# Optimization experiments

Hardware: AMD Instinct MI355X
Metric: run time of the kernel (lower is better)

Reference implementation:

```python
import jax, jax.numpy as jnp
import numpy as np

EMBED_DIM = 768
NUM_HEADS = 12
HEAD_DIM = EMBED_DIM // NUM_HEADS
SCALE = HEAD_DIM ** -0.5


def setup_inputs() -> dict:
    key = jax.random.key(0)
    k1, k2, k3, k4, k5 = jax.random.split(key, 5)
    B, T = 8, 1024
    init = 0.02
    return {
        "hidden_states": jax.random.normal(k1, (B, T, EMBED_DIM), dtype=jnp.float32),
        "qkv_w": jax.random.normal(k2, (EMBED_DIM, 3 * EMBED_DIM), dtype=jnp.float32) * init,
        "qkv_b": jnp.zeros((3 * EMBED_DIM,), dtype=jnp.float32),
        "proj_w": jax.random.normal(k3, (EMBED_DIM, EMBED_DIM), dtype=jnp.float32) * init,
        "proj_b": jnp.zeros((EMBED_DIM,), dtype=jnp.float32),
    }


def reference(hidden_states, qkv_w, qkv_b, proj_w, proj_b):
    B, T, E = hidden_states.shape
    # fused QKV projection: [B, T, 3E] -> [3, B, H, T, Dh]
    mixed = hidden_states @ qkv_w + qkv_b
    mixed = mixed.reshape(B, T, 3, NUM_HEADS, HEAD_DIM).transpose(2, 0, 3, 1, 4)
    q, k, v = mixed[0], mixed[1], mixed[2]
    # scores: [B, H, T, T]
    scores = jnp.einsum("bhqd,bhkd->bhqk", q, k) * SCALE
    probs = jax.nn.softmax(scores, axis=-1)
    # context: [B, T, H, Dh] -> [B, T, E]
    ctx = jnp.einsum("bhqk,bhkd->bqhd", probs, v).reshape(B, T, E)
    return ctx @ proj_w + proj_b
```

## Files before the change

### kernel.cpp

```cpp
#include <hip/hip_runtime.h>
#include <hip/hip_bf16.h>

#define B_ 8
#define T_ 1024
#define E_ 768
#define H_ 12
#define DH_ 64
#define E3_ 2304
#define M_ (B_ * T_)
#define SCALE_LOG2E 0.18033688011112042f

typedef __attribute__((ext_vector_type(8))) short short8;
typedef __attribute__((ext_vector_type(4))) float float4_;
typedef __attribute__((ext_vector_type(4))) unsigned short ushort4_;

__device__ __forceinline__ unsigned short f2bf(float f) {
    union { float f; unsigned int u; } v; v.f = f;
    unsigned int r = v.u + 0x7fffu + ((v.u >> 16) & 1u);
    return (unsigned short)(r >> 16);
}

__device__ __forceinline__ unsigned int pk_bf16(float a, float b) {
    float2 t; t.x = a; t.y = b;
    union { __hip_bfloat162 h; unsigned int u; } cv;
    cv.h = __float22bfloat162_rn(t);
    return cv.u;
}

__device__ __forceinline__ void gld_lds16(const unsigned short* g, unsigned short* l) {
    __builtin_amdgcn_global_load_lds(
        (const __attribute__((address_space(1))) void*)g,
        (__attribute__((address_space(3))) void*)l,
        16, 0, 0);
}

__global__ __launch_bounds__(256) void prep(const float* __restrict__ hs,
                                            const float* __restrict__ qkv_w,
                                            const float* __restrict__ proj_w,
                                            unsigned short* __restrict__ hs_bf,
                                            unsigned short* __restrict__ qkvwT,
                                            unsigned short* __restrict__ projwT) {
    __shared__ float tile[32][33];
    const int id = blockIdx.x;
    const int tid = threadIdx.x;
    if (id < 6144) {
        const int i = (id * 256 + tid) * 4;
        float4_ v = *(const float4_*)(hs + i);
        ushort4_ o;
        o.x = f2bf(v.x); o.y = f2bf(v.y); o.z = f2bf(v.z); o.w = f2bf(v.w);
        *(ushort4_*)(hs_bf + i) = o;
        return;
    }
    const float* W; unsigned short* Wt; int N, bx, by;
    if (id < 6144 + 1728) {
        const int t = id - 6144; W = qkv_w; Wt = qkvwT; N = E3_;
        bx = t % 72; by = t / 72;
    } else {
        const int t = id - 7872; W = proj_w; Wt = projwT; N = E_;
        bx = t % 24; by = t / 24;
    }
    const int k0 = by * 32, n0 = bx * 32;
    const int tx = tid & 31, ty = tid >> 5;
    for (int i = ty; i < 32; i += 8)
        tile[i][tx] = W[(size_t)(k0 + i) * N + n0 + tx];
    __syncthreads();
    for (int i = ty; i < 32; i += 8)
        Wt[(size_t)(n0 + i) * E_ + k0 + tx] = f2bf(tile[tx][i]);
}

template <int STORE_MODE>
__global__ __launch_bounds__(256) void gemm_mfma(const unsigned short* __restrict__ A,
                                                 const unsigned short* __restrict__ Wt,
                                                 const float* __restrict__ bias,
                                                 void* __restrict__ Cout,
                                                 unsigned short* __restrict__ Vt,
                                                 int M, int N, int K) {
    __shared__ __align__(16) unsigned short Al[2][128 * 32];
    __shared__ __align__(16) unsigned short Wl[2][128 * 32];

    const int tid = threadIdx.x;
    const int lane = tid & 63;
    const int w = tid >> 6;

    const int id = blockIdx.x;
    const int xcd = id & 7;
    const int slot = id >> 3;
    const int bx = slot >> 3;
    const int by = xcd * 8 + (slot & 7);
    const int bm = by * 128;
    const int bn = bx * 128;

    const int wm = (w >> 1) * 64;
    const int wn = (w & 1) * 64;
    const int quad = lane >> 4;
    const int l16 = lane & 15;

    const int srow = w * 32 + (lane >> 2);
    const int schunk = (lane & 3) * 8;
    const int sbase = w * 32 * 32 + lane * 8;

    const unsigned short* ga = A + (size_t)(bm + srow) * K + schunk;
    const unsigned short* gw = Wt + (size_t)(bn + srow) * K + schunk;

    float4_ acc[4][4] = {};

    gld_lds16(ga, &Al[0][sbase]);
    gld_lds16(ga + (size_t)16 * K, &Al[0][sbase + 512]);
    gld_lds16(gw, &Wl[0][sbase]);
    gld_lds16(gw + (size_t)16 * K, &Wl[0][sbase + 512]);

    const int NI = K >> 5;
    for (int i = 0; i < NI; ++i) {
        const int cur = i & 1;
        __syncthreads();
        if (i + 1 < NI) {
            const unsigned short* ga2 = ga + (size_t)(i + 1) * 32;
            const unsigned short* gw2 = gw + (size_t)(i + 1) * 32;
            const int nxt = cur ^ 1;
            gld_lds16(ga2, &Al[nxt][sbase]);
            gld_lds16(ga2 + (size_t)16 * K, &Al[nxt][sbase + 512]);
            gld_lds16(gw2, &Wl[nxt][sbase]);
            gld_lds16(gw2 + (size_t)16 * K, &Wl[nxt][sbase + 512]);
        }
        short8 af[4], bf[4];
#pragma unroll
        for (int mt = 0; mt < 4; ++mt)
            af[mt] = *(const short8*)(&Al[cur][(wm + mt * 16 + l16) * 32 + quad * 8]);
#pragma unroll
        for (int nt = 0; nt < 4; ++nt)
            bf[nt] = *(const short8*)(&Wl[cur][(wn + nt * 16 + l16) * 32 + quad * 8]);
#pragma unroll
        for (int mt = 0; mt < 4; ++mt)
#pragma unroll
            for (int nt = 0; nt < 4; ++nt)
                acc[mt][nt] = __builtin_amdgcn_mfma_f32_16x16x32_bf16(af[mt], bf[nt],
                                                                      acc[mt][nt], 0, 0, 0);
    }

    {
#pragma unroll
        for (int nt = 0; nt < 4; ++nt) {
            const int col = bn + wn + nt * 16 + l16;
            const float bv = bias[col];
#pragma unroll
            for (int mt = 0; mt < 4; ++mt) {
#pragma unroll
                for (int i = 0; i < 4; ++i) {
                    const int row = bm + wm + mt * 16 + quad * 4 + i;
                    const float v = acc[mt][nt][i] + bv;
                    if (STORE_MODE >= 1)
                        ((unsigned short*)Cout)[(size_t)row * N + col] = f2bf(v);
                    else
                        ((float*)Cout)[(size_t)row * N + col] = v;
                }
            }
        }
    }
    (void)Vt;
}

__global__ __launch_bounds__(512, 2) void gemm288(const unsigned short* __restrict__ A,
                                                  const unsigned short* __restrict__ Wt,
                                                  const float* __restrict__ bias,
                                                  unsigned short* __restrict__ mixedOut,
                                                  unsigned short* __restrict__ Vt) {
    const int K = 768;
    const int NT = 12;
    __shared__ __align__(16) unsigned short lds[70144];

    const int tid = threadIdx.x;
    const int lane = tid & 63;
    const int w = tid >> 6;
    const int quad = lane >> 4;
    const int l16 = lane & 15;
    const int wM = w >> 1;
    const int wN = w & 1;

    const int id = blockIdx.x;
    const int xcd = id & 7;
    const int slot = id >> 3;
    const int bx = slot >> 2;
    const int byl = slot & 3;
    const int bm = (xcd * 4 + byl) * 256;
    const int bn = bx * 288;

    const int j4 = (w < 4) ? (w + 32) : 36;
    int kk0 = ((w % 18) / 6) * 64 + w;
    int kk1 = (((w + 8) % 18) / 6) * 64 + (w + 8);
    int kk2 = (((w + 16) % 18) / 6) * 64 + (w + 16);
    int kk3 = (((w + 24) % 18) / 6) * 64 + (w + 24);
    int kk4 = (j4 >= 36) ? (3 * 64 + 36) : (((j4 % 18) / 6) * 64 + j4);
#define CS_(a, b) { int _lo = min(a, b), _hi = max(a, b); a = _lo; b = _hi; }
    CS_(kk0, kk1) CS_(kk3, kk4) CS_(kk2, kk4) CS_(kk2, kk3) CS_(kk1, kk4)
    CS_(kk0, kk3) CS_(kk0, kk2) CS_(kk1, kk3) CS_(kk1, kk2)
#undef CS_
    const int b0 = kk0 & 63, b1 = kk1 & 63, b2 = kk2 & 63, b3 = kk3 & 63, b4 = kk4 & 63;

    const int srcrow = lane >> 3;
    const int ssw = ((lane & 7) ^ (srcrow & 7)) << 3;
    const unsigned short* gaL = A + (size_t)(bm + srcrow) * K + ssw;
    const unsigned short* gbL = Wt + (size_t)(bn + srcrow) * K + ssw;
    unsigned short* ldsl = lds + lane * 8;

    const int rsw0 = ((quad) ^ (l16 & 7)) << 3;
    const int rsw1 = ((quad + 4) ^ (l16 & 7)) << 3;
    const unsigned short* rdA = lds + (wM * 64 + l16) * 64;
    const unsigned short* rdB = lds + 32768 + (wN * 144 + l16) * 64;

    short8 aF[4][2], bF[3][2];
    float4_ acc[4][9] = {};

#define STA_(aj, toff, bufA) gld_lds16(gaL + (size_t)(aj) * 6144 + (toff), (bufA) + (aj) * 512)
#define STB_(j, toff, bufB) { \
    const int _j = (j); \
    const unsigned short* _s = gbL + (size_t)(_j >= 36 ? 0 : _j) * 6144 + (toff); \
    unsigned short* _d = (_j >= 36) ? (ldsl + 69632) : ((bufB) + _j * 512); \
    gld_lds16(_s, _d); }

#define LDA_(buf) { \
    const unsigned short* _a = rdA + (buf) * 16384; \
    aF[0][0] = *(const short8*)(_a + rsw0);        aF[0][1] = *(const short8*)(_a + rsw1); \
    aF[1][0] = *(const short8*)(_a + 1024 + rsw0); aF[1][1] = *(const short8*)(_a + 1024 + rsw1); \
    aF[2][0] = *(const short8*)(_a + 2048 + rsw0); aF[2][1] = *(const short8*)(_a + 2048 + rsw1); \
    aF[3][0] = *(const short8*)(_a + 3072 + rsw0); aF[3][1] = *(const short8*)(_a + 3072 + rsw1); }

#define LDB_(buf, nh) { \
    const unsigned short* _b = rdB + (buf) * 18432 + (nh) * 3072; \
    bF[0][0] = *(const short8*)(_b + rsw0);        bF[0][1] = *(const short8*)(_b + rsw1); \
    bF[1][0] = *(const short8*)(_b + 1024 + rsw0); bF[1][1] = *(const short8*)(_b + 1024 + rsw1); \
    bF[2][0] = *(const short8*)(_b + 2048 + rsw0); bF[2][1] = *(const short8*)(_b + 2048 + rsw1); }

#define MMA_(nh) \
    __builtin_amdgcn_s_setprio(1); \
    _Pragma("unroll") for (int mt = 0; mt < 4; ++mt) \
    _Pragma("unroll") for (int nt = 0; nt < 3; ++nt) { \
        acc[mt][(nh) * 3 + nt] = __builtin_amdgcn_mfma_f32_16x16x32_bf16( \
            aF[mt][0], bF[nt][0], acc[mt][(nh) * 3 + nt], 0, 0, 0); \
        acc[mt][(nh) * 3 + nt] = __builtin_amdgcn_mfma_f32_16x16x32_bf16( \
            aF[mt][1], bF[nt][1], acc[mt][(nh) * 3 + nt], 0, 0, 0); } \
    __builtin_amdgcn_s_setprio(0);

#define BARRIER_ __builtin_amdgcn_s_barrier()
#define WLGKM0_ { asm volatile("s_waitcnt lgkmcnt(0)" ::: "memory"); __builtin_amdgcn_sched_barrier(0); }
#define WVM3_ asm volatile("s_waitcnt vmcnt(3)" ::: "memory")
#define WVM0_ asm volatile("s_waitcnt vmcnt(0)" ::: "memory")

    {
        unsigned short* bufA = ldsl;
        unsigned short* bufB = ldsl + 32768;
        STA_(w, 0, bufA); STA_(w + 8, 0, bufA); STA_(w + 16, 0, bufA); STA_(w + 24, 0, bufA);
        STB_(b0, 0, bufB); STB_(b1, 0, bufB); STB_(b2, 0, bufB); STB_(b3, 0, bufB); STB_(b4, 0, bufB);
    }
    WVM3_; BARRIER_;

#pragma unroll 1
    for (int t = 0; t < NT - 1; ++t) {
        const int buf = t & 1;
        const int toff = (t + 1) * 64;
        unsigned short* bufA = ldsl + (buf ^ 1) * 16384;
        unsigned short* bufB = ldsl + 32768 + (buf ^ 1) * 18432;

        LDA_(buf); LDB_(buf, 0);
        STA_(w, toff, bufA); STA_(w + 8, toff, bufA); STA_(w + 16, toff, bufA);
        BARRIER_; WLGKM0_; MMA_(0);
        WVM3_; BARRIER_;
        LDB_(buf, 1);
        STA_(w + 24, toff, bufA); STB_(b0, toff, bufB); STB_(b1, toff, bufB);
        BARRIER_; WLGKM0_; MMA_(1);
        WVM3_; BARRIER_;
        LDB_(buf, 2);
        STB_(b2, toff, bufB); STB_(b3, toff, bufB); STB_(b4, toff, bufB);
        BARRIER_; WLGKM0_; MMA_(2);
        WVM3_; BARRIER_;
    }
    {
        LDA_(1); LDB_(1, 0);
        BARRIER_; WLGKM0_; MMA_(0);
        WVM0_; BARRIER_;
        LDB_(1, 1);
        BARRIER_; WLGKM0_; MMA_(1);
        BARRIER_;
        LDB_(1, 2);
        BARRIER_; WLGKM0_; MMA_(2);
    }
#undef STA_
#undef STB_
#undef LDA_
#undef LDB_
#undef MMA_

    const int bb = bm >> 10;
    const int tloc = (bm & 1023) + wM * 64;
#pragma unroll
    for (int ntg = 0; ntg < 9; ++ntg) {
        const int col = bn + wN * 144 + ntg * 16 + l16;
        const float bv = bias[col];
        if (col >= 1536) {
            const int n = col - 1536;
            const int h = n >> 6, d = n & 63;
            const size_t vrow = (size_t)((bb * H_ + h) * 64 + d) * T_;
#pragma unroll
            for (int mt = 0; mt < 4; ++mt) {
                uint2 pk;
                pk.x = pk_bf16(acc[mt][ntg][0] + bv, acc[mt][ntg][1] + bv);
                pk.y = pk_bf16(acc[mt][ntg][2] + bv, acc[mt][ntg][3] + bv);
                *(uint2*)(Vt + vrow + tloc + mt * 16 + quad * 4) = pk;
            }
        } else {
            const float qs = (col < 768) ? SCALE_LOG2E : 1.0f;
#pragma unroll
            for (int mt = 0; mt < 4; ++mt) {
#pragma unroll
                for (int i = 0; i < 4; ++i) {
                    const int row = bm + wM * 64 + mt * 16 + quad * 4 + i;
                    mixedOut[(size_t)row * E3_ + col] = f2bf((acc[mt][ntg][i] + bv) * qs);
                }
            }
        }
    }
}

__global__ __launch_bounds__(256) void attn_mfma(const unsigned short* __restrict__ mixed,
                                                 const unsigned short* __restrict__ Vt,
                                                 unsigned short* __restrict__ ctx) {
    const int bh = blockIdx.x;
    const int b = bh / H_;
    const int h = bh % H_;
    const int q0 = blockIdx.y * 128;
    const int tid = threadIdx.x;
    const int lane = tid & 63;
    const int w = tid >> 6;
    const int quad = lane >> 4;
    const int l16 = lane & 15;

    __shared__ __align__(16) unsigned short Kl[8 * 520];
    __shared__ __align__(16) unsigned short Vl[8 * 520];
    __shared__ __align__(16) unsigned short Pl[4][32 * 72];
    unsigned short* pw = &Pl[w][0];

    short8 qf[2][2];
#pragma unroll
    for (int hh = 0; hh < 2; ++hh) {
        const size_t qrow = (size_t)(b * T_ + q0 + w * 32 + hh * 16 + l16) * E3_ + h * 64;
        qf[hh][0] = *(const short8*)(mixed + qrow + quad * 8);
        qf[hh][1] = *(const short8*)(mixed + qrow + 32 + quad * 8);
    }

    float4_ o[2][4] = {};
    float lps[2] = {0.0f, 0.0f};

    const size_t kbase = (size_t)(b * T_) * E3_ + E_ + h * 64;
    const size_t vtb = (size_t)bh * 64 * T_;

    const int srow = tid >> 3;
    const int sc = tid & 7;

    short8 k1 = *(const short8*)(mixed + kbase + (size_t)srow * E3_ + sc * 8);
    short8 k2 = *(const short8*)(mixed + kbase + (size_t)(srow + 32) * E3_ + sc * 8);
    short8 v1 = *(const short8*)(Vt + vtb + (size_t)srow * T_ + sc * 8);
    short8 v2 = *(const short8*)(Vt + vtb + (size_t)(srow + 32) * T_ + sc * 8);

    for (int kv0 = 0; kv0 < T_; kv0 += 64) {
        __syncthreads();
        *(short8*)(&Kl[sc * 520 + srow * 8]) = k1;
        *(short8*)(&Kl[sc * 520 + (srow + 32) * 8]) = k2;
        *(short8*)(&Vl[sc * 520 + srow * 8]) = v1;
        *(short8*)(&Vl[sc * 520 + (srow + 32) * 8]) = v2;
        __syncthreads();

        if (kv0 + 64 < T_) {
            const int kn = kv0 + 64;
            k1 = *(const short8*)(mixed + kbase + (size_t)(kn + srow) * E3_ + sc * 8);
            k2 = *(const short8*)(mixed + kbase + (size_t)(kn + srow + 32) * E3_ + sc * 8);
            v1 = *(const short8*)(Vt + vtb + (size_t)srow * T_ + kn + sc * 8);
            v2 = *(const short8*)(Vt + vtb + (size_t)(srow + 32) * T_ + kn + sc * 8);
        }

        float4_ st[2][4];
#pragma unroll
        for (int nt = 0; nt < 4; ++nt) {
            const int key = nt * 16 + l16;
            short8 kf0 = *(const short8*)(&Kl[quad * 520 + key * 8]);
            short8 kf1 = *(const short8*)(&Kl[(4 + quad) * 520 + key * 8]);
#pragma unroll
            for (int hh = 0; hh < 2; ++hh) {
                float4_ z = {};
                z = __builtin_amdgcn_mfma_f32_16x16x32_bf16(kf0, qf[hh][0], z, 0, 0, 0);
                st[hh][nt] = __builtin_amdgcn_mfma_f32_16x16x32_bf16(kf1, qf[hh][1], z, 0, 0, 0);
            }
        }

#pragma unroll
        for (int hh = 0; hh < 2; ++hh) {
#pragma unroll
            for (int nt = 0; nt < 4; ++nt) {
                const float p0 = __builtin_amdgcn_exp2f(st[hh][nt][0]);
                const float p1 = __builtin_amdgcn_exp2f(st[hh][nt][1]);
                const float p2 = __builtin_amdgcn_exp2f(st[hh][nt][2]);
                const float p3 = __builtin_amdgcn_exp2f(st[hh][nt][3]);
                uint2 pk;
                pk.x = pk_bf16(p0, p1);
                pk.y = pk_bf16(p2, p3);
                lps[hh] += (p0 + p1) + (p2 + p3);
                *(uint2*)(&pw[(hh * 16 + l16) * 72 + nt * 16 + quad * 4]) = pk;
            }
        }

        short8 pf[2][2];
#pragma unroll
        for (int hh = 0; hh < 2; ++hh) {
            pf[hh][0] = *(const short8*)(&pw[(hh * 16 + l16) * 72 + quad * 8]);
            pf[hh][1] = *(const short8*)(&pw[(hh * 16 + l16) * 72 + 32 + quad * 8]);
        }

#pragma unroll
        for (int dt = 0; dt < 4; ++dt) {
            const int d = dt * 16 + l16;
            short8 vf0 = *(const short8*)(&Vl[quad * 520 + d * 8]);
            short8 vf1 = *(const short8*)(&Vl[(4 + quad) * 520 + d * 8]);
#pragma unroll
            for (int hh = 0; hh < 2; ++hh) {
                o[hh][dt] = __builtin_amdgcn_mfma_f32_16x16x32_bf16(pf[hh][0], vf0, o[hh][dt], 0, 0, 0);
                o[hh][dt] = __builtin_amdgcn_mfma_f32_16x16x32_bf16(pf[hh][1], vf1, o[hh][dt], 0, 0, 0);
            }
        }
    }

#pragma unroll
    for (int hh = 0; hh < 2; ++hh) {
        float l = lps[hh];
        l += __shfl_xor(l, 16, 64);
        l += __shfl_xor(l, 32, 64);
        float4_ inv;
#pragma unroll
        for (int i = 0; i < 4; ++i)
            inv[i] = 1.0f / __shfl(l, quad * 4 + i, 16);
#pragma unroll
        for (int dt = 0; dt < 4; ++dt) {
#pragma unroll
            for (int i = 0; i < 4; ++i) {
                const float v = o[hh][dt][i] * inv[i];
                const size_t row = (size_t)(b * T_ + q0 + w * 32 + hh * 16 + quad * 4 + i);
                ctx[row * E_ + h * 64 + dt * 16 + l16] = f2bf(v);
            }
        }
    }
}

extern "C" void kernel_launch(void* const* d_in, const int* in_sizes, int n_in,
                              void* d_out, int out_size, void* d_ws, size_t ws_size,
                              hipStream_t stream) {
    const float* hs     = (const float*)d_in[0];
    const float* qkv_w  = (const float*)d_in[1];
    const float* qkv_b  = (const float*)d_in[2];
    const float* proj_w = (const float*)d_in[3];
    const float* proj_b = (const float*)d_in[4];
    float* out = (float*)d_out;

    unsigned short* hs_bf  = (unsigned short*)d_ws;
    unsigned short* qkvwT  = hs_bf + (size_t)M_ * E_;
    unsigned short* projwT = qkvwT + (size_t)E3_ * E_;
    unsigned short* mixed  = projwT + (size_t)E_ * E_;
    unsigned short* Vt     = mixed + (size_t)M_ * E3_;
    unsigned short* ctx    = hs_bf;

    prep<<<8448, 256, 0, stream>>>(hs, qkv_w, proj_w, hs_bf, qkvwT, projwT);

    gemm288<<<256, 512, 0, stream>>>(hs_bf, qkvwT, qkv_b, mixed, Vt);
    attn_mfma<<<dim3(B_ * H_, T_ / 128), 256, 0, stream>>>(mixed, Vt, ctx);
    gemm_mfma<0><<<(E_ / 128) * (M_ / 128), 256, 0, stream>>>(ctx, projwT, proj_b,
                                                              (void*)out, nullptr, M_, E_, E_);
}
```

Before: 179.8 us.

## Switch attention to 32x32x16 MFMA and keep P in registers via permlane swap

Rewrites the attention inner loop to use 32x32x16 bf16 MFMAs, computing S^T so that each lane holds probabilities for one query column. The P tile is converted to the A-operand layout in registers with v_permlane32_swap instead of a round trip through shared memory, which removes the per-wave P buffer and its LDS writes and reads. This cuts LDS traffic and instruction count. In exchange it relies on exact register layout correctness for the swap and changes the epilogue's row mapping.

```diff
diff --git a/kernel.cpp b/kernel.cpp
--- a/kernel.cpp
+++ b/kernel.cpp
@@ -12,6 +12,7 @@
 
 typedef __attribute__((ext_vector_type(8))) short short8;
 typedef __attribute__((ext_vector_type(4))) float float4_;
+typedef __attribute__((ext_vector_type(16))) float f32x16;
 typedef __attribute__((ext_vector_type(4))) unsigned short ushort4_;
 
 __device__ __forceinline__ unsigned short f2bf(float f) {
@@ -25,6 +26,10 @@
     union { __hip_bfloat162 h; unsigned int u; } cv;
     cv.h = __float22bfloat162_rn(t);
     return cv.u;
+}
+
+__device__ __forceinline__ void pl32swap(unsigned int& a, unsigned int& b) {
+    asm volatile("v_permlane32_swap_b32 %0, %1" : "+v"(a), "+v"(b));
 }
 
 __device__ __forceinline__ void gld_lds16(const unsigned short* g, unsigned short* l) {
@@ -330,24 +335,23 @@
     const int tid = threadIdx.x;
     const int lane = tid & 63;
     const int w = tid >> 6;
-    const int quad = lane >> 4;
-    const int l16 = lane & 15;
+    const int l32 = lane & 31;
+    const int hi = lane >> 5;
 
     __shared__ __align__(16) unsigned short Kl[8 * 520];
     __shared__ __align__(16) unsigned short Vl[8 * 520];
-    __shared__ __align__(16) unsigned short Pl[4][32 * 72];
-    unsigned short* pw = &Pl[w][0];
-
-    short8 qf[2][2];
-#pragma unroll
-    for (int hh = 0; hh < 2; ++hh) {
-        const size_t qrow = (size_t)(b * T_ + q0 + w * 32 + hh * 16 + l16) * E3_ + h * 64;
-        qf[hh][0] = *(const short8*)(mixed + qrow + quad * 8);
-        qf[hh][1] = *(const short8*)(mixed + qrow + 32 + quad * 8);
-    }
-
-    float4_ o[2][4] = {};
-    float lps[2] = {0.0f, 0.0f};
+
+    short8 qB[4];
+    {
+        const size_t qrow = (size_t)(b * T_ + q0 + w * 32 + l32) * E3_ + h * 64;
+#pragma unroll
+        for (int dc = 0; dc < 4; ++dc)
+            qB[dc] = *(const short8*)(mixed + qrow + dc * 16 + hi * 8);
+    }
+
+    f32x16 o0 = {};
+    f32x16 o1 = {};
+    float lps = 0.0f;
 
     const size_t kbase = (size_t)(b * T_) * E3_ + E_ + h * 64;
     const size_t vtb = (size_t)bh * 64 * T_;
@@ -376,74 +380,63 @@
             v2 = *(const short8*)(Vt + vtb + (size_t)(srow + 32) * T_ + kn + sc * 8);
         }
 
-        float4_ st[2][4];
-#pragma unroll
-        for (int nt = 0; nt < 4; ++nt) {
-            const int key = nt * 16 + l16;
-            short8 kf0 = *(const short8*)(&Kl[quad * 520 + key * 8]);
-            short8 kf1 = *(const short8*)(&Kl[(4 + quad) * 520 + key * 8]);
-#pragma unroll
-            for (int hh = 0; hh < 2; ++hh) {
-                float4_ z = {};
-                z = __builtin_amdgcn_mfma_f32_16x16x32_bf16(kf0, qf[hh][0], z, 0, 0, 0);
-                st[hh][nt] = __builtin_amdgcn_mfma_f32_16x16x32_bf16(kf1, qf[hh][1], z, 0, 0, 0);
-            }
+#pragma unroll
+        for (int kg = 0; kg < 2; ++kg) {
+            short8 kf0 = *(const short8*)(&Kl[(0 + hi) * 520 + (kg * 32 + l32) * 8]);
+            short8 kf1 = *(const short8*)(&Kl[(2 + hi) * 520 + (kg * 32 + l32) * 8]);
+            short8 kf2 = *(const short8*)(&Kl[(4 + hi) * 520 + (kg * 32 + l32) * 8]);
+            short8 kf3 = *(const short8*)(&Kl[(6 + hi) * 520 + (kg * 32 + l32) * 8]);
+
+            f32x16 st = {};
+            st = __builtin_amdgcn_mfma_f32_32x32x16_bf16(kf0, qB[0], st, 0, 0, 0);
+            st = __builtin_amdgcn_mfma_f32_32x32x16_bf16(kf1, qB[1], st, 0, 0, 0);
+            st = __builtin_amdgcn_mfma_f32_32x32x16_bf16(kf2, qB[2], st, 0, 0, 0);
+            st = __builtin_amdgcn_mfma_f32_32x32x16_bf16(kf3, qB[3], st, 0, 0, 0);
+
+            float e[16];
+#pragma unroll
+            for (int r = 0; r < 16; ++r)
+                e[r] = __builtin_amdgcn_exp2f(st[r]);
+            lps += ((((e[0] + e[1]) + (e[2] + e[3])) + ((e[4] + e[5]) + (e[6] + e[7]))) +
+                    (((e[8] + e[9]) + (e[10] + e[11])) + ((e[12] + e[13]) + (e[14] + e[15]))));
+
+            unsigned int u0 = pk_bf16(e[0], e[1]);
+            unsigned int u1 = pk_bf16(e[2], e[3]);
+            unsigned int u2 = pk_bf16(e[4], e[5]);
+            unsigned int u3 = pk_bf16(e[6], e[7]);
+            pl32swap(u0, u2);
+            pl32swap(u1, u3);
+            unsigned int u4 = pk_bf16(e[8], e[9]);
+            unsigned int u5 = pk_bf16(e[10], e[11]);
+            unsigned int u6 = pk_bf16(e[12], e[13]);
+            unsigned int u7 = pk_bf16(e[14], e[15]);
+            pl32swap(u4, u6);
+            pl32swap(u5, u7);
+            union { unsigned int u[4]; short8 s; } pa0, pa1;
+            pa0.u[0] = u0; pa0.u[1] = u1; pa0.u[2] = u2; pa0.u[3] = u3;
+            pa1.u[0] = u4; pa1.u[1] = u5; pa1.u[2] = u6; pa1.u[3] = u7;
+
+            short8 vb00 = *(const short8*)(&Vl[(kg * 4 + 0 + hi) * 520 + l32 * 8]);
+            short8 vb01 = *(const short8*)(&Vl[(kg * 4 + 0 + hi) * 520 + (32 + l32) * 8]);
+            short8 vb10 = *(const short8*)(&Vl[(kg * 4 + 2 + hi) * 520 + l32 * 8]);
+            short8 vb11 = *(const short8*)(&Vl[(kg * 4 + 2 + hi) * 520 + (32 + l32) * 8]);
+
+            o0 = __builtin_amdgcn_mfma_f32_32x32x16_bf16(pa0.s, vb00, o0, 0, 0, 0);
+            o1 = __builtin_amdgcn_mfma_f32_32x32x16_bf16(pa0.s, vb01, o1, 0, 0, 0);
+            o0 = __builtin_amdgcn_mfma_f32_32x32x16_bf16(pa1.s, vb10, o0, 0, 0, 0);
+            o1 = __builtin_amdgcn_mfma_f32_32x32x16_bf16(pa1.s, vb11, o1, 0, 0, 0);
         }
-
-#pragma unroll
-        for (int hh = 0; hh < 2; ++hh) {
-#pragma unroll
-            for (int nt = 0; nt < 4; ++nt) {
-                const float p0 = __builtin_amdgcn_exp2f(st[hh][nt][0]);
-                const float p1 = __builtin_amdgcn_exp2f(st[hh][nt][1]);
-                const float p2 = __builtin_amdgcn_exp2f(st[hh][nt][2]);
-                const float p3 = __builtin_amdgcn_exp2f(st[hh][nt][3]);
-                uint2 pk;
-                pk.x = pk_bf16(p0, p1);
-                pk.y = pk_bf16(p2, p3);
-                lps[hh] += (p0 + p1) + (p2 + p3);
-                *(uint2*)(&pw[(hh * 16 + l16) * 72 + nt * 16 + quad * 4]) = pk;
-            }
-        }
-
-        short8 pf[2][2];
-#pragma unroll
-        for (int hh = 0; hh < 2; ++hh) {
-            pf[hh][0] = *(const short8*)(&pw[(hh * 16 + l16) * 72 + quad * 8]);
-            pf[hh][1] = *(const short8*)(&pw[(hh * 16 + l16) * 72 + 32 + quad * 8]);
-        }
-
-#pragma unroll
-        for (int dt = 0; dt < 4; ++dt) {
-            const int d = dt * 16 + l16;
-            short8 vf0 = *(const short8*)(&Vl[quad * 520 + d * 8]);
-            short8 vf1 = *(const short8*)(&Vl[(4 + quad) * 520 + d * 8]);
-#pragma unroll
-            for (int hh = 0; hh < 2; ++hh) {
-                o[hh][dt] = __builtin_amdgcn_mfma_f32_16x16x32_bf16(pf[hh][0], vf0, o[hh][dt], 0, 0, 0);
-                o[hh][dt] = __builtin_amdgcn_mfma_f32_16x16x32_bf16(pf[hh][1], vf1, o[hh][dt], 0, 0, 0);
-            }
-        }
-    }
-
-#pragma unroll
-    for (int hh = 0; hh < 2; ++hh) {
-        float l = lps[hh];
-        l += __shfl_xor(l, 16, 64);
-        l += __shfl_xor(l, 32, 64);
-        float4_ inv;
-#pragma unroll
-        for (int i = 0; i < 4; ++i)
-            inv[i] = 1.0f / __shfl(l, quad * 4 + i, 16);
-#pragma unroll
-        for (int dt = 0; dt < 4; ++dt) {
-#pragma unroll
-            for (int i = 0; i < 4; ++i) {
-                const float v = o[hh][dt][i] * inv[i];
-                const size_t row = (size_t)(b * T_ + q0 + w * 32 + hh * 16 + quad * 4 + i);
-                ctx[row * E_ + h * 64 + dt * 16 + l16] = f2bf(v);
-            }
-        }
+    }
+
+    const float lt = lps + __shfl_xor(lps, 32, 64);
+    const float invq = 1.0f / lt;
+#pragma unroll
+    for (int r = 0; r < 16; ++r) {
+        const int row = (r & 3) + 8 * (r >> 2) + 4 * hi;
+        const float iv = __shfl(invq, row, 32);
+        const size_t orow = (size_t)(b * T_ + q0 + w * 32 + row) * E_ + h * 64 + l32;
+        ctx[orow] = f2bf(o0[r] * iv);
+        ctx[orow + 32] = f2bf(o1[r] * iv);
     }
 }
 
```

Result: no change. 180.2 us (+0.2%).

## Replace output projection GEMM with 256x96-tiled pipelined kernel

Applied to the files above, without the earlier changes.

Replaces the generic 128x128 double-buffered output-projection GEMM with a dedicated kernel that uses 256x96 tiles, 512 threads and K-steps of 64. It adds XOR-swizzled LDS layout, staged async global-to-LDS loads interleaved with MFMA phases, and s_setprio around the MFMA bursts. The grid shrinks to 256 blocks, about one per CU, to cut wave-quantization and tail effects from the earlier 384-block launch. The cost is more complex hand-scheduled synchronization and higher register and LDS pressure.

```diff
diff --git a/kernel.cpp b/kernel.cpp
--- a/kernel.cpp
+++ b/kernel.cpp
@@ -68,97 +68,6 @@
         Wt[(size_t)(n0 + i) * E_ + k0 + tx] = f2bf(tile[tx][i]);
 }
 
-template <int STORE_MODE>
-__global__ __launch_bounds__(256) void gemm_mfma(const unsigned short* __restrict__ A,
-                                                 const unsigned short* __restrict__ Wt,
-                                                 const float* __restrict__ bias,
-                                                 void* __restrict__ Cout,
-                                                 unsigned short* __restrict__ Vt,
-                                                 int M, int N, int K) {
-    __shared__ __align__(16) unsigned short Al[2][128 * 32];
-    __shared__ __align__(16) unsigned short Wl[2][128 * 32];
-
-    const int tid = threadIdx.x;
-    const int lane = tid & 63;
-    const int w = tid >> 6;
-
-    const int id = blockIdx.x;
-    const int xcd = id & 7;
-    const int slot = id >> 3;
-    const int bx = slot >> 3;
-    const int by = xcd * 8 + (slot & 7);
-    const int bm = by * 128;
-    const int bn = bx * 128;
-
-    const int wm = (w >> 1) * 64;
-    const int wn = (w & 1) * 64;
-    const int quad = lane >> 4;
-    const int l16 = lane & 15;
-
-    const int srow = w * 32 + (lane >> 2);
-    const int schunk = (lane & 3) * 8;
-    const int sbase = w * 32 * 32 + lane * 8;
-
-    const unsigned short* ga = A + (size_t)(bm + srow) * K + schunk;
-    const unsigned short* gw = Wt + (size_t)(bn + srow) * K + schunk;
-
-    float4_ acc[4][4] = {};
-
-    gld_lds16(ga, &Al[0][sbase]);
-    gld_lds16(ga + (size_t)16 * K, &Al[0][sbase + 512]);
-    gld_lds16(gw, &Wl[0][sbase]);
-    gld_lds16(gw + (size_t)16 * K, &Wl[0][sbase + 512]);
-
-    const int NI = K >> 5;
-    for (int i = 0; i < NI; ++i) {
-        const int cur = i & 1;
-        __syncthreads();
-        if (i + 1 < NI) {
-            const unsigned short* ga2 = ga + (size_t)(i + 1) * 32;
-            const unsigned short* gw2 = gw + (size_t)(i + 1) * 32;
-            const int nxt = cur ^ 1;
-            gld_lds16(ga2, &Al[nxt][sbase]);
-            gld_lds16(ga2 + (size_t)16 * K, &Al[nxt][sbase + 512]);
-            gld_lds16(gw2, &Wl[nxt][sbase]);
-            gld_lds16(gw2 + (size_t)16 * K, &Wl[nxt][sbase + 512]);
-        }
-        short8 af[4], bf[4];
-#pragma unroll
-        for (int mt = 0; mt < 4; ++mt)
-            af[mt] = *(const short8*)(&Al[cur][(wm + mt * 16 + l16) * 32 + quad * 8]);
-#pragma unroll
-        for (int nt = 0; nt < 4; ++nt)
-            bf[nt] = *(const short8*)(&Wl[cur][(wn + nt * 16 + l16) * 32 + quad * 8]);
-#pragma unroll
-        for (int mt = 0; mt < 4; ++mt)
-#pragma unroll
-            for (int nt = 0; nt < 4; ++nt)
-                acc[mt][nt] = __builtin_amdgcn_mfma_f32_16x16x32_bf16(af[mt], bf[nt],
-                                                                      acc[mt][nt], 0, 0, 0);
-    }
-
-    {
-#pragma unroll
-        for (int nt = 0; nt < 4; ++nt) {
-            const int col = bn + wn + nt * 16 + l16;
-            const float bv = bias[col];
-#pragma unroll
-            for (int mt = 0; mt < 4; ++mt) {
-#pragma unroll
-                for (int i = 0; i < 4; ++i) {
-                    const int row = bm + wm + mt * 16 + quad * 4 + i;
-                    const float v = acc[mt][nt][i] + bv;
-                    if (STORE_MODE >= 1)
-                        ((unsigned short*)Cout)[(size_t)row * N + col] = f2bf(v);
-                    else
-                        ((float*)Cout)[(size_t)row * N + col] = v;
-                }
-            }
-        }
-    }
-    (void)Vt;
-}
-
 __global__ __launch_bounds__(512, 2) void gemm288(const unsigned short* __restrict__ A,
                                                   const unsigned short* __restrict__ Wt,
                                                   const float* __restrict__ bias,
@@ -320,6 +229,124 @@
     }
 }
 
+__global__ __launch_bounds__(512, 2) void proj96(const unsigned short* __restrict__ A,
+                                                 const unsigned short* __restrict__ Wt,
+                                                 const float* __restrict__ bias,
+                                                 float* __restrict__ out) {
+    const int K = 768;
+    const int NT = 12;
+    __shared__ __align__(16) unsigned short lds[45568];
+
+    const int tid = threadIdx.x;
+    const int lane = tid & 63;
+    const int w = tid >> 6;
+    const int quad = lane >> 4;
+    const int l16 = lane & 15;
+    const int wM = w >> 1;
+    const int wN = w & 1;
+
+    const int id = blockIdx.x;
+    const int xcd = id & 7;
+    const int slot = id >> 3;
+    const int bx = slot >> 2;
+    const int byl = slot & 3;
+    const int bm = (xcd * 4 + byl) * 256;
+    const int bn = bx * 96;
+
+    const int jB2 = (w < 4) ? (8 + w) : -1;
+
+    const int srcrow = lane >> 3;
+    const int ssw = ((lane & 7) ^ (srcrow & 7)) << 3;
+    const unsigned short* gaL = A + (size_t)(bm + srcrow) * K + ssw;
+    const unsigned short* gbL = Wt + (size_t)(bn + srcrow) * K + ssw;
+    unsigned short* ldsl = lds + lane * 8;
+
+    const int rsw0 = ((quad) ^ (l16 & 7)) << 3;
+    const int rsw1 = ((quad + 4) ^ (l16 & 7)) << 3;
+    const unsigned short* rdA = lds + (wM * 64 + l16) * 64;
+    const unsigned short* rdB = lds + 32768 + (wN * 48 + l16) * 64;
+
+    short8 aF[4][2], bF[2];
+    float4_ acc[4][3] = {};
+
+#define PSTA(aj, toff, nb) gld_lds16(gaL + (size_t)(aj) * 6144 + (toff), \
+                                     ldsl + (nb) * 16384 + (aj) * 512)
+#define PSTB(j, toff, nb) { \
+    const int _j = (j); \
+    const unsigned short* _s = gbL + (size_t)(_j < 0 ? 0 : _j) * 6144 + (toff); \
+    unsigned short* _d = (_j < 0) ? (ldsl + 45056) : (ldsl + 32768 + (nb) * 6144 + _j * 512); \
+    gld_lds16(_s, _d); }
+#define PLDA(buf) { \
+    const unsigned short* _a = rdA + (buf) * 16384; \
+    aF[0][0] = *(const short8*)(_a + rsw0);        aF[0][1] = *(const short8*)(_a + rsw1); \
+    aF[1][0] = *(const short8*)(_a + 1024 + rsw0); aF[1][1] = *(const short8*)(_a + 1024 + rsw1); \
+    aF[2][0] = *(const short8*)(_a + 2048 + rsw0); aF[2][1] = *(const short8*)(_a + 2048 + rsw1); \
+    aF[3][0] = *(const short8*)(_a + 3072 + rsw0); aF[3][1] = *(const short8*)(_a + 3072 + rsw1); }
+#define PLDB(buf, nt_) { \
+    const unsigned short* _b = rdB + (buf) * 6144 + (nt_) * 1024; \
+    bF[0] = *(const short8*)(_b + rsw0); \
+    bF[1] = *(const short8*)(_b + rsw1); }
+#define PMMA(nt_) \
+    __builtin_amdgcn_s_setprio(1); \
+    _Pragma("unroll") for (int mt = 0; mt < 4; ++mt) { \
+        acc[mt][nt_] = __builtin_amdgcn_mfma_f32_16x16x32_bf16(aF[mt][0], bF[0], acc[mt][nt_], 0, 0, 0); \
+        acc[mt][nt_] = __builtin_amdgcn_mfma_f32_16x16x32_bf16(aF[mt][1], bF[1], acc[mt][nt_], 0, 0, 0); } \
+    __builtin_amdgcn_s_setprio(0);
+#define PBAR __builtin_amdgcn_s_barrier()
+#define PLGKM0 { asm volatile("s_waitcnt lgkmcnt(0)" ::: "memory"); __builtin_amdgcn_sched_barrier(0); }
+
+    PSTA(w, 0, 0); PSTA(w + 8, 0, 0); PSTA(w + 16, 0, 0); PSTA(w + 24, 0, 0);
+    PSTB(w, 0, 0); PSTB(jB2, 0, 0);
+    asm volatile("s_waitcnt vmcnt(0)" ::: "memory");
+    PBAR;
+
+#pragma unroll 1
+    for (int t = 0; t < NT - 1; ++t) {
+        const int buf = t & 1;
+        const int nb = buf ^ 1;
+        const int toff = (t + 1) * 64;
+
+        PLDA(buf); PLDB(buf, 0);
+        PSTA(w, toff, nb); PSTA(w + 8, toff, nb); PSTA(w + 16, toff, nb);
+        PBAR; PLGKM0; PMMA(0);
+        asm volatile("s_waitcnt vmcnt(3)" ::: "memory"); PBAR;
+        PLDB(buf, 1);
+        PSTA(w + 24, toff, nb); PSTB(w, toff, nb); PSTB(jB2, toff, nb);
+        PBAR; PLGKM0; PMMA(1);
+        asm volatile("s_waitcnt vmcnt(3)" ::: "memory"); PBAR;
+        PLDB(buf, 2);
+        PBAR; PLGKM0; PMMA(2);
+        asm volatile("s_waitcnt vmcnt(0)" ::: "memory"); PBAR;
+    }
+    {
+        PLDA(1);
+        PLDB(1, 0); PLGKM0; PMMA(0);
+        PLDB(1, 1); PLGKM0; PMMA(1);
+        PLDB(1, 2); PLGKM0; PMMA(2);
+    }
+#undef PSTA
+#undef PSTB
+#undef PLDA
+#undef PLDB
+#undef PMMA
+#undef PBAR
+#undef PLGKM0
+
+#pragma unroll
+    for (int nt = 0; nt < 3; ++nt) {
+        const int col = bn + wN * 48 + nt * 16 + l16;
+        const float bv = bias[col];
+#pragma unroll
+        for (int mt = 0; mt < 4; ++mt) {
+#pragma unroll
+            for (int i = 0; i < 4; ++i) {
+                const int row = bm + wM * 64 + mt * 16 + quad * 4 + i;
+                out[(size_t)row * E_ + col] = acc[mt][nt][i] + bv;
+            }
+        }
+    }
+}
+
 __global__ __launch_bounds__(256) void attn_mfma(const unsigned short* __restrict__ mixed,
                                                  const unsigned short* __restrict__ Vt,
                                                  unsigned short* __restrict__ ctx) {
@@ -468,6 +495,5 @@
 
     gemm288<<<256, 512, 0, stream>>>(hs_bf, qkvwT, qkv_b, mixed, Vt);
     attn_mfma<<<dim3(B_ * H_, T_ / 128), 256, 0, stream>>>(mixed, Vt, ctx);
-    gemm_mfma<0><<<(E_ / 128) * (M_ / 128), 256, 0, stream>>>(ctx, projwT, proj_b,
-                                                              (void*)out, nullptr, M_, E_, E_);
-}
+    proj96<<<256, 512, 0, stream>>>(ctx, projwT, proj_b, out);
+}
```

After: 176.6 us. Within noise of the previous version (-1.8%).
